# Kernel tuning notes

Measured on AMD Instinct MI355X. Metric: run time of the kernel, lower is better.

Reference implementation:

```python
import jax, jax.numpy as jnp
import numpy as np

N, F, H, E = 100000, 128, 128, 3200000
EPS = 1e-5


def setup_inputs() -> dict:
    key = jax.random.key(0)
    ks = jax.random.split(key, 16)
    g = lambda k, shape, fan_in: jax.random.normal(k, shape, jnp.float32) / np.sqrt(fan_in)
    inp = {
        'x': jax.random.normal(ks[0], (N, F), jnp.float32),
        'edge_index': jax.random.randint(ks[1], (2, E), 0, N, jnp.int64),
        # SAGEConv params: lin_l (aggregated-neighbor path, has bias), lin_r (root path, no bias)
        'W1l': g(ks[2], (F, H), F), 'b1': jnp.zeros((H,), jnp.float32), 'W1r': g(ks[3], (F, H), F),
        'W2l': g(ks[4], (H, H), H), 'b2': jnp.zeros((H,), jnp.float32), 'W2r': g(ks[5], (H, H), H),
        'W3l': g(ks[6], (H, H), H), 'b3': jnp.zeros((H,), jnp.float32), 'W3r': g(ks[7], (H, H), H),
        'W4l': g(ks[8], (H, 1), H), 'b4': jnp.zeros((1,), jnp.float32), 'W4r': g(ks[9], (H, 1), H),
        # BatchNorm affine params
        'g1': jnp.ones((H,), jnp.float32), 'be1': jnp.zeros((H,), jnp.float32),
        'g2': jnp.ones((H,), jnp.float32), 'be2': jnp.zeros((H,), jnp.float32),
        'g3': jnp.ones((H,), jnp.float32), 'be3': jnp.zeros((H,), jnp.float32),
        # shared residual linear
        'Wlin': g(ks[10], (H, H), H), 'blin': jnp.zeros((H,), jnp.float32),
    }
    return inp


def _sage(x, src, dst, Wl, b, Wr):
    # mean aggregation of source features at destination nodes
    n = x.shape[0]
    s = jax.ops.segment_sum(x[src], dst, num_segments=n)          # [N, d]
    cnt = jax.ops.segment_sum(jnp.ones_like(dst, x.dtype), dst, num_segments=n)
    agg = s / jnp.maximum(cnt, 1.0)[:, None]
    return agg @ Wl + b + x @ Wr


def _bn(x, gamma, beta):
    # training-mode batch norm over node dim (biased variance, as torch)
    mu = x.mean(0)
    var = jnp.mean((x - mu) ** 2, axis=0)
    return gamma * (x - mu) * jax.lax.rsqrt(var + EPS) + beta


def reference(x, edge_index, W1l, b1, W1r, W2l, b2, W2r, W3l, b3, W3r,
              W4l, b4, W4r, g1, be1, g2, be2, g3, be3, Wlin, blin):
    src, dst = edge_index[0], edge_index[1]
    # dropout is identity (eval-mode reference)
    x1 = jax.nn.elu(_bn(_sage(x, src, dst, W1l, b1, W1r), g1, be1))
    x2 = jax.nn.elu(_bn(_sage(x1, src, dst, W2l, b2, W2r), g2, be2))
    x2 = x2 + x1 @ Wlin + blin
    x3 = jax.nn.elu(_bn(_sage(x2, src, dst, W3l, b3, W3r), g3, be3))
    x3 = x3 + x2 @ Wlin + blin
    x4 = _sage(x3, src, dst, W4l, b4, W4r)  # [N, 1]
    return jnp.squeeze(x4, -1)
```

## Files before the change

### kernel.cpp

```cpp
#include <hip/hip_runtime.h>
#include <hip/hip_bf16.h>
#include <math.h>

#define BN_EPS 1e-5f
#define BSTRIDE 96

typedef __attribute__((ext_vector_type(8))) short bf16x8;
typedef __attribute__((ext_vector_type(4))) float f32x4;
typedef unsigned int uint32;

__device__ __forceinline__ unsigned bf16rne(float f) {
  unsigned u = __float_as_uint(f);
  unsigned r = u + 0x7fffu + ((u >> 16) & 1u);
  return r >> 16;
}
__device__ __forceinline__ float bf2f_lo(uint32 u) { return __uint_as_float(u << 16); }
__device__ __forceinline__ float bf2f_hi(uint32 u) { return __uint_as_float(u & 0xffff0000u); }
__device__ __forceinline__ uint32 packbf2(float a, float b) {
  return bf16rne(a) | (bf16rne(b) << 16);
}

__device__ __forceinline__ int edge_at(const int* __restrict__ ei, long long idx, int is64) {
  return is64 ? ei[2 * idx] : ei[idx];
}

__global__ void detect_kernel(const int* __restrict__ ei, long long E, int* __restrict__ flag) {
  __shared__ int found;
  int t = threadIdx.x;
  if (t == 0) found = 0;
  __syncthreads();
  long long npairs = E < 1024 ? E : 1024;
  for (long long p = t; p < npairs; p += blockDim.x)
    if (ei[2 * p + 1] != 0) found = 1;
  __syncthreads();
  if (t == 0) *flag = found ? 0 : 1;
}

__launch_bounds__(256)
__global__ void build_kernel(const int* __restrict__ ei, long long E,
                             const int* __restrict__ flag,
                             int* __restrict__ cnt, int* __restrict__ bkt,
                             const float* __restrict__ x, uint32* __restrict__ xb,
                             long long nf4,
                             const float* __restrict__ Wa, const float* __restrict__ Wb,
                             const float* __restrict__ Wc, const float* __restrict__ Wd,
                             const float* __restrict__ We, const float* __restrict__ Wf,
                             const float* __restrict__ Wg, ushort* __restrict__ Wp,
                             long long K3) {
  long long b = blockIdx.x;
  if (b >= K3) {
    int rb = (int)(b - K3);
    int wi = rb >> 3;
    const float* W = wi == 0 ? Wa : wi == 1 ? Wb : wi == 2 ? Wc : wi == 3 ? Wd
                   : wi == 4 ? We : wi == 5 ? Wf : Wg;
    ushort* dst = Wp + (size_t)wi * 16384;
    int s = (rb & 7) * 256 + threadIdx.x;
    int nt = s >> 8, rem = s & 255, ks = rem >> 6, lane = rem & 63;
    int q = lane >> 4, l16 = lane & 15;
    int kbase = ks * 32 + q * 8, c = nt * 16 + l16;
    uint32 o[4];
#pragma unroll
    for (int jp = 0; jp < 4; ++jp) {
      float fa = W[(size_t)(kbase + 2 * jp) * 128 + c];
      float fb = W[(size_t)(kbase + 2 * jp + 1) * 128 + c];
      o[jp] = packbf2(fa, fb);
    }
    ((uint4*)dst)[s] = make_uint4(o[0], o[1], o[2], o[3]);
    return;
  }
  int role = (int)(b % 3);
  long long id = b / 3;
  if (role == 0) {
    long long g = id * 256 + threadIdx.x;
    long long e0 = 2 * g;
    if (e0 >= E) return;
    int is64 = *flag;
    bool h1 = (e0 + 1 < E);
    int s0, s1 = 0, d0, d1 = 0;
    if (is64 && !(E & 1)) {
      int4 sv = ((const int4*)ei)[g];
      int4 dv = ((const int4*)(ei + 2 * E))[g];
      s0 = sv.x; s1 = sv.z;
      d0 = dv.x; d1 = dv.z;
    } else {
      s0 = edge_at(ei, e0, is64);
      d0 = edge_at(ei, E + e0, is64);
      if (h1) {
        s1 = edge_at(ei, e0 + 1, is64);
        d1 = edge_at(ei, E + e0 + 1, is64);
      }
    }
    int r0 = atomicAdd(&cnt[d0], 1);
    if (r0 < BSTRIDE) bkt[(size_t)d0 * BSTRIDE + r0] = s0;
    if (h1) {
      int r1 = atomicAdd(&cnt[d1], 1);
      if (r1 < BSTRIDE) bkt[(size_t)d1 * BSTRIDE + r1] = s1;
    }
  } else {
    long long i = (id * 2 + (role - 1)) * 256 + threadIdx.x;
    if (i < nf4) {
      float4 f = ((const float4*)x)[i];
      uint2 o2;
      o2.x = packbf2(f.x, f.y);
      o2.y = packbf2(f.z, f.w);
      ((uint2*)xb)[i] = o2;
    }
  }
}

__global__ void aggregate_bf16_kernel(const uint32* __restrict__ X, const int* __restrict__ cnt,
                                      const int* __restrict__ bkt, uint32* __restrict__ out,
                                      int N) {
  int gw = (int)((blockIdx.x * (long long)blockDim.x + threadIdx.x) >> 6);
  int lane = threadIdx.x & 63;
  if (gw >= N) return;
  int deg = cnt[gw];
  if (deg > BSTRIDE) deg = BSTRIDE;
  int b = gw * BSTRIDE, e = b + deg;
  int sub = lane & 15, grp = lane >> 4;
  const uint4* X4 = (const uint4*)X;
  float acc[8];
#pragma unroll
  for (int j = 0; j < 8; ++j) acc[j] = 0.f;
  for (int i = b; i < e; i += 32) {
    uint4 v[8];
#pragma unroll
    for (int u = 0; u < 8; ++u) {
      int ii = i + u * 4 + grp;
      v[u] = make_uint4(0, 0, 0, 0);
      if (ii < e) { int s = bkt[ii]; v[u] = X4[(size_t)s * 16 + sub]; }
    }
#pragma unroll
    for (int u = 0; u < 8; ++u) {
      acc[0] += bf2f_lo(v[u].x); acc[1] += bf2f_hi(v[u].x);
      acc[2] += bf2f_lo(v[u].y); acc[3] += bf2f_hi(v[u].y);
      acc[4] += bf2f_lo(v[u].z); acc[5] += bf2f_hi(v[u].z);
      acc[6] += bf2f_lo(v[u].w); acc[7] += bf2f_hi(v[u].w);
    }
  }
#pragma unroll
  for (int j = 0; j < 8; ++j) {
    acc[j] += __shfl_xor(acc[j], 16, 64);
    acc[j] += __shfl_xor(acc[j], 32, 64);
  }
  if (grp == 0) {
    float inv = 1.0f / fmaxf((float)deg, 1.0f);
    uint4 o;
    o.x = packbf2(acc[0] * inv, acc[1] * inv);
    o.y = packbf2(acc[2] * inv, acc[3] * inv);
    o.z = packbf2(acc[4] * inv, acc[5] * inv);
    o.w = packbf2(acc[6] * inv, acc[7] * inv);
    ((uint4*)out)[(size_t)gw * 16 + sub] = o;
  }
}

template <int HR>
__launch_bounds__(256)
__global__ void gemm_mfma_kernel(const ushort* __restrict__ A1, const ushort* __restrict__ W1p,
                                 const ushort* __restrict__ A2, const ushort* __restrict__ W2p,
                                 const ushort* __restrict__ W3p,
                                 const float* __restrict__ bias, const float* __restrict__ rbias,
                                 ushort* __restrict__ Y, ushort* __restrict__ R,
                                 float* __restrict__ bnsum, int N) {
  __shared__ float sred[16][128];
  int t = threadIdx.x;
  int w = t >> 6, lane = t & 63;
  int quad = lane >> 4, l16 = lane & 15;
  int row0 = blockIdx.x * 64 + w * 16;

  f32x4 accY[8], accR[HR ? 8 : 1];
#pragma unroll
  for (int nt = 0; nt < 8; ++nt) {
    accY[nt][0] = accY[nt][1] = accY[nt][2] = accY[nt][3] = 0.f;
    if (HR) {
      accR[nt][0] = accR[nt][1] = accR[nt][2] = accR[nt][3] = 0.f;
    }
  }

  int rowA = row0 + l16;
  if (rowA > N - 1) rowA = N - 1;
  const ushort* a1p = A1 + (size_t)rowA * 128 + quad * 8;
  const ushort* a2p = A2 + (size_t)rowA * 128 + quad * 8;

#pragma unroll
  for (int ks = 0; ks < 4; ++ks) {
    bf16x8 a = *(const bf16x8*)(a1p + ks * 32);
#pragma unroll
    for (int nt = 0; nt < 8; ++nt) {
      bf16x8 b = *(const bf16x8*)(W1p + ((size_t)(nt * 4 + ks) * 64 + lane) * 8);
      accY[nt] = __builtin_amdgcn_mfma_f32_16x16x32_bf16(a, b, accY[nt], 0, 0, 0);
    }
  }
#pragma unroll
  for (int ks = 0; ks < 4; ++ks) {
    bf16x8 a = *(const bf16x8*)(a2p + ks * 32);
#pragma unroll
    for (int nt = 0; nt < 8; ++nt) {
      bf16x8 b = *(const bf16x8*)(W2p + ((size_t)(nt * 4 + ks) * 64 + lane) * 8);
      accY[nt] = __builtin_amdgcn_mfma_f32_16x16x32_bf16(a, b, accY[nt], 0, 0, 0);
    }
    if (HR) {
#pragma unroll
      for (int nt = 0; nt < 8; ++nt) {
        bf16x8 b = *(const bf16x8*)(W3p + ((size_t)(nt * 4 + ks) * 64 + lane) * 8);
        accR[nt] = __builtin_amdgcn_mfma_f32_16x16x32_bf16(a, b, accR[nt], 0, 0, 0);
      }
    }
  }

  float s1v[8], s2v[8];
#pragma unroll
  for (int nt = 0; nt < 8; ++nt) {
    int c = nt * 16 + l16;
    float bv = bias[c];
    float rb = HR ? rbias[c] : 0.f;
    s1v[nt] = 0.f; s2v[nt] = 0.f;
#pragma unroll
    for (int reg = 0; reg < 4; ++reg) {
      int grow = row0 + quad * 4 + reg;
      if (grow < N) {
        float v = accY[nt][reg] + bv;
        Y[(size_t)grow * 128 + c] = (ushort)bf16rne(v);
        s1v[nt] += v; s2v[nt] += v * v;
        if (HR) {
          float vr = accR[nt][reg] + rb;
          R[(size_t)grow * 128 + c] = (ushort)bf16rne(vr);
        }
      }
    }
  }

  int rrow = w * 4 + quad;
#pragma unroll
  for (int nt = 0; nt < 8; ++nt) sred[rrow][nt * 16 + l16] = s1v[nt];
  __syncthreads();
  if (t < 128) {
    float tot = 0.f;
#pragma unroll
    for (int r16 = 0; r16 < 16; ++r16) tot += sred[r16][t];
    atomicAdd(&bnsum[(size_t)(blockIdx.x & 63) * 256 + t], tot);
  }
  __syncthreads();
#pragma unroll
  for (int nt = 0; nt < 8; ++nt) sred[rrow][nt * 16 + l16] = s2v[nt];
  __syncthreads();
  if (t < 128) {
    float tot = 0.f;
#pragma unroll
    for (int r16 = 0; r16 < 16; ++r16) tot += sred[r16][t];
    atomicAdd(&bnsum[(size_t)(blockIdx.x & 63) * 256 + 128 + t], tot);
  }
}

__global__ void bn_finalize_kernel(float* __restrict__ bnsum, float* __restrict__ bnp, int N) {
  __shared__ float part[256];
  int t = threadIdx.x;
  float a0 = 0.f, a1 = 0.f, a2 = 0.f, a3 = 0.f;
#pragma unroll
  for (int sh = 0; sh < 64; sh += 4) {
    a0 += bnsum[(size_t)(sh + 0) * 256 + t];
    a1 += bnsum[(size_t)(sh + 1) * 256 + t];
    a2 += bnsum[(size_t)(sh + 2) * 256 + t];
    a3 += bnsum[(size_t)(sh + 3) * 256 + t];
  }
  part[t] = (a0 + a1) + (a2 + a3);
  __syncthreads();
  if (t < 128) {
    float invN = 1.0f / (float)N;
    float mu = part[t] * invN;
    float var = part[128 + t] * invN - mu * mu;
    bnp[t] = mu;
    bnp[128 + t] = rsqrtf(var + BN_EPS);
  }
  __syncthreads();
  for (int i = t; i < 64 * 256; i += 256) bnsum[i] = 0.f;
}

__global__ void bn_elu_kernel(const uint4* __restrict__ Y4, const float* __restrict__ bnp,
                              const float* __restrict__ g, const float* __restrict__ be,
                              const uint4* __restrict__ res4, uint4* __restrict__ Xo4,
                              const float* __restrict__ W4l, const float* __restrict__ W4r,
                              float* __restrict__ z, float* __restrict__ rr,
                              long long total4) {
  long long i = blockIdx.x * (long long)blockDim.x + threadIdx.x;
  if (i >= total4) return;
  int c0 = (int)(i & 15) * 8;
  uint4 y = Y4[i];
  float v[8];
  {
    uint32 ww[4] = {y.x, y.y, y.z, y.w};
#pragma unroll
    for (int j = 0; j < 4; ++j) {
      int c = c0 + 2 * j;
      float e0 = g[c]     * (bf2f_lo(ww[j]) - bnp[c])     * bnp[128 + c]     + be[c];
      float e1 = g[c + 1] * (bf2f_hi(ww[j]) - bnp[c + 1]) * bnp[128 + c + 1] + be[c + 1];
      v[2 * j]     = e0 > 0.f ? e0 : expm1f(e0);
      v[2 * j + 1] = e1 > 0.f ? e1 : expm1f(e1);
    }
  }
  if (res4) {
    uint4 rv = res4[i];
    uint32 ww[4] = {rv.x, rv.y, rv.z, rv.w};
#pragma unroll
    for (int j = 0; j < 4; ++j) {
      v[2 * j]     += bf2f_lo(ww[j]);
      v[2 * j + 1] += bf2f_hi(ww[j]);
    }
  }
  if (Xo4) {
    uint4 o;
    o.x = packbf2(v[0], v[1]);
    o.y = packbf2(v[2], v[3]);
    o.z = packbf2(v[4], v[5]);
    o.w = packbf2(v[6], v[7]);
    Xo4[i] = o;
  }
  if (z) {
    float a = 0.f, bb = 0.f;
#pragma unroll
    for (int j = 0; j < 8; ++j) {
      a  += v[j] * W4l[c0 + j];
      bb += v[j] * W4r[c0 + j];
    }
    a  += __shfl_xor(a, 1, 64);  bb += __shfl_xor(bb, 1, 64);
    a  += __shfl_xor(a, 2, 64);  bb += __shfl_xor(bb, 2, 64);
    a  += __shfl_xor(a, 4, 64);  bb += __shfl_xor(bb, 4, 64);
    a  += __shfl_xor(a, 8, 64);  bb += __shfl_xor(bb, 8, 64);
    if ((i & 15) == 0) {
      long long row = i >> 4;
      z[row] = a;
      rr[row] = bb;
    }
  }
}

__global__ void final_kernel(const float* __restrict__ z, const float* __restrict__ rr,
                             const int* __restrict__ cnt, const int* __restrict__ bkt,
                             const float* __restrict__ b4, float* __restrict__ out, int N) {
  long long t = blockIdx.x * (long long)blockDim.x + threadIdx.x;
  int n = (int)(t >> 3);
  int q = (int)(t & 7);
  if (n >= N) n = N - 1;
  int deg = cnt[n];
  if (deg > BSTRIDE) deg = BSTRIDE;
  int b = n * BSTRIDE, e = b + deg;
  float s = 0.f;
  for (int i = b + q; i < e; i += 8) s += z[bkt[i]];
  s += __shfl_xor(s, 1, 64);
  s += __shfl_xor(s, 2, 64);
  s += __shfl_xor(s, 4, 64);
  if (q == 0) out[n] = s / fmaxf((float)deg, 1.0f) + b4[0] + rr[n];
}

extern "C" void kernel_launch(void* const* d_in, const int* in_sizes, int n_in,
                              void* d_out, int out_size, void* d_ws, size_t ws_size,
                              hipStream_t stream) {
  const float* x   = (const float*)d_in[0];
  const int*   ei  = (const int*)d_in[1];
  const float* W1l = (const float*)d_in[2];
  const float* b1  = (const float*)d_in[3];
  const float* W1r = (const float*)d_in[4];
  const float* W2l = (const float*)d_in[5];
  const float* b2  = (const float*)d_in[6];
  const float* W2r = (const float*)d_in[7];
  const float* W3l = (const float*)d_in[8];
  const float* b3  = (const float*)d_in[9];
  const float* W3r = (const float*)d_in[10];
  const float* W4l = (const float*)d_in[11];
  const float* b4  = (const float*)d_in[12];
  const float* W4r = (const float*)d_in[13];
  const float* g1  = (const float*)d_in[14];
  const float* be1 = (const float*)d_in[15];
  const float* g2  = (const float*)d_in[16];
  const float* be2 = (const float*)d_in[17];
  const float* g3  = (const float*)d_in[18];
  const float* be3 = (const float*)d_in[19];
  const float* Wlin= (const float*)d_in[20];
  const float* blin= (const float*)d_in[21];

  const int N = in_sizes[0] / 128;
  const long long E = in_sizes[1] / 2;
  float* out = (float*)d_out;

  const int B = 256;
  const int gb = (N + 63) / 64;

  char* w = (char*)d_ws;
  size_t o = 0;
  auto alloc = [&](size_t bytes) -> char* {
    char* p = w + o;
    o = (o + bytes + 255) & ~(size_t)255;
    return p;
  };
  int*      cnt   = (int*)alloc((size_t)N * 4);
  int*      flag  = (int*)alloc(4);
  float*    bnsum = (float*)alloc((size_t)64 * 256 * 4);
  float*    bnp   = (float*)alloc(256 * 4);
  float*    z     = (float*)alloc((size_t)N * 4);
  float*    rr    = (float*)alloc((size_t)N * 4);
  ushort*   Wp    = (ushort*)alloc((size_t)7 * 2048 * 16);
  int*      bkt   = (int*)alloc((size_t)N * BSTRIDE * 4);
  char* B1c = alloc((size_t)N * 256);
  char* B2c = alloc((size_t)N * 256);
  char* B3c = alloc((size_t)N * 256);
  (void)ws_size; (void)n_in; (void)out_size;

  uint32* B1 = (uint32*)B1c;
  uint32* B2 = (uint32*)B2c;
  uint32* B3 = (uint32*)B3c;

  const long long pairs = (E + 1) / 2;
  const int ebp = (int)((pairs + B - 1) / B);
  const long long nf4 = (long long)N * 32;
  const int cb4 = (int)((nf4 + B - 1) / B);
  int K = ebp > (cb4 + 1) / 2 ? ebp : (cb4 + 1) / 2;
  const int Gbuild = 3 * K + 56;
  const int wb = (int)(((long long)N * 64 + B - 1) / B);
  const long long tot4 = (long long)N * 16;
  const int cb = (int)((tot4 + B - 1) / B);
  const int fb = (int)(((long long)N * 8 + B - 1) / B);

  ushort* Wp1l = Wp + 0 * 16384;
  ushort* Wp1r = Wp + 1 * 16384;
  ushort* Wp2l = Wp + 2 * 16384;
  ushort* Wp2r = Wp + 3 * 16384;
  ushort* Wp3l = Wp + 4 * 16384;
  ushort* Wp3r = Wp + 5 * 16384;
  ushort* Wpln = Wp + 6 * 16384;

  hipMemsetAsync(cnt, 0, (size_t)N * 4, stream);
  hipMemsetAsync(bnsum, 0, (size_t)64 * 256 * 4, stream);
  detect_kernel<<<1, 1024, 0, stream>>>(ei, E, flag);
  build_kernel<<<Gbuild, B, 0, stream>>>(ei, E, flag, cnt, bkt, x, B2, nf4,
                                         W1l, W1r, W2l, W2r, W3l, W3r, Wlin, Wp,
                                         (long long)3 * K);

  aggregate_bf16_kernel<<<wb, B, 0, stream>>>(B2, cnt, bkt, B1, N);
  gemm_mfma_kernel<0><<<gb, B, 0, stream>>>((const ushort*)B1, Wp1l, (const ushort*)B2, Wp1r,
                                            nullptr, b1, nullptr, (ushort*)B1, nullptr,
                                            bnsum, N);
  bn_finalize_kernel<<<1, 256, 0, stream>>>(bnsum, bnp, N);
  bn_elu_kernel<<<cb, B, 0, stream>>>((const uint4*)B1, bnp, g1, be1, nullptr, (uint4*)B3,
                                      nullptr, nullptr, nullptr, nullptr, tot4);

  aggregate_bf16_kernel<<<wb, B, 0, stream>>>(B3, cnt, bkt, B1, N);
  gemm_mfma_kernel<1><<<gb, B, 0, stream>>>((const ushort*)B1, Wp2l, (const ushort*)B3, Wp2r,
                                            Wpln, b2, blin, (ushort*)B1, (ushort*)B2,
                                            bnsum, N);
  bn_finalize_kernel<<<1, 256, 0, stream>>>(bnsum, bnp, N);
  bn_elu_kernel<<<cb, B, 0, stream>>>((const uint4*)B1, bnp, g2, be2, (const uint4*)B2,
                                      (uint4*)B2, nullptr, nullptr, nullptr, nullptr, tot4);

  aggregate_bf16_kernel<<<wb, B, 0, stream>>>(B2, cnt, bkt, B1, N);
  gemm_mfma_kernel<1><<<gb, B, 0, stream>>>((const ushort*)B1, Wp3l, (const ushort*)B2, Wp3r,
                                            Wpln, b3, blin, (ushort*)B1, (ushort*)B3,
                                            bnsum, N);
  bn_finalize_kernel<<<1, 256, 0, stream>>>(bnsum, bnp, N);
  bn_elu_kernel<<<cb, B, 0, stream>>>((const uint4*)B1, bnp, g3, be3, (const uint4*)B3,
                                      nullptr, W4l, W4r, z, rr, tot4);

  final_kernel<<<fb, B, 0, stream>>>(z, rr, cnt, bkt, b4, out, N);
}
```

Measured before the change: 846.7 us.

## Fuse neighbor mean aggregation into the MFMA GEMM via swizzled LDS tile

Removes the separate aggregation kernel. Each wave of the GEMM kernel now gathers and averages neighbor features for its 16 rows and writes the bf16 means into a swizzled shared-memory tile, which feeds the MFMA A operand directly. This drops the global write and read of the aggregated matrix and three kernel launches per run, and merges the two memsets into one by reordering workspace allocation. The trade-off is less latency hiding: each wave aggregates its 16 nodes one after another before its GEMM work, with fewer waves in flight and extra LDS use, so the irregular gather may be exposed.

After: 1.252 ms. 47.9% more time.

```diff
diff --git a/kernel.cpp b/kernel.cpp
--- a/kernel.cpp
+++ b/kernel.cpp
@@ -108,66 +108,66 @@
   }
 }
 
-__global__ void aggregate_bf16_kernel(const uint32* __restrict__ X, const int* __restrict__ cnt,
-                                      const int* __restrict__ bkt, uint32* __restrict__ out,
-                                      int N) {
-  int gw = (int)((blockIdx.x * (long long)blockDim.x + threadIdx.x) >> 6);
-  int lane = threadIdx.x & 63;
-  if (gw >= N) return;
-  int deg = cnt[gw];
-  if (deg > BSTRIDE) deg = BSTRIDE;
-  int b = gw * BSTRIDE, e = b + deg;
-  int sub = lane & 15, grp = lane >> 4;
-  const uint4* X4 = (const uint4*)X;
-  float acc[8];
-#pragma unroll
-  for (int j = 0; j < 8; ++j) acc[j] = 0.f;
-  for (int i = b; i < e; i += 32) {
-    uint4 v[8];
-#pragma unroll
-    for (int u = 0; u < 8; ++u) {
-      int ii = i + u * 4 + grp;
-      v[u] = make_uint4(0, 0, 0, 0);
-      if (ii < e) { int s = bkt[ii]; v[u] = X4[(size_t)s * 16 + sub]; }
-    }
-#pragma unroll
-    for (int u = 0; u < 8; ++u) {
-      acc[0] += bf2f_lo(v[u].x); acc[1] += bf2f_hi(v[u].x);
-      acc[2] += bf2f_lo(v[u].y); acc[3] += bf2f_hi(v[u].y);
-      acc[4] += bf2f_lo(v[u].z); acc[5] += bf2f_hi(v[u].z);
-      acc[6] += bf2f_lo(v[u].w); acc[7] += bf2f_hi(v[u].w);
-    }
-  }
-#pragma unroll
-  for (int j = 0; j < 8; ++j) {
-    acc[j] += __shfl_xor(acc[j], 16, 64);
-    acc[j] += __shfl_xor(acc[j], 32, 64);
-  }
-  if (grp == 0) {
-    float inv = 1.0f / fmaxf((float)deg, 1.0f);
-    uint4 o;
-    o.x = packbf2(acc[0] * inv, acc[1] * inv);
-    o.y = packbf2(acc[2] * inv, acc[3] * inv);
-    o.z = packbf2(acc[4] * inv, acc[5] * inv);
-    o.w = packbf2(acc[6] * inv, acc[7] * inv);
-    ((uint4*)out)[(size_t)gw * 16 + sub] = o;
-  }
-}
-
 template <int HR>
 __launch_bounds__(256)
-__global__ void gemm_mfma_kernel(const ushort* __restrict__ A1, const ushort* __restrict__ W1p,
-                                 const ushort* __restrict__ A2, const ushort* __restrict__ W2p,
-                                 const ushort* __restrict__ W3p,
-                                 const float* __restrict__ bias, const float* __restrict__ rbias,
-                                 ushort* __restrict__ Y, ushort* __restrict__ R,
-                                 float* __restrict__ bnsum, int N) {
+__global__ void gemm_fused_kernel(const uint32* __restrict__ X, const int* __restrict__ cnt,
+                                  const int* __restrict__ bkt,
+                                  const ushort* __restrict__ W1p, const ushort* __restrict__ W2p,
+                                  const ushort* __restrict__ W3p,
+                                  const float* __restrict__ bias, const float* __restrict__ rbias,
+                                  ushort* __restrict__ Y, ushort* __restrict__ R,
+                                  float* __restrict__ bnsum, int N) {
   __shared__ float sred[16][128];
+  __shared__ uint32 atile[4][16 * 64];
   int t = threadIdx.x;
   int w = t >> 6, lane = t & 63;
   int quad = lane >> 4, l16 = lane & 15;
   int row0 = blockIdx.x * 64 + w * 16;
 
+  const uint4* X4 = (const uint4*)X;
+  for (int n = 0; n < 16; ++n) {
+    int node = row0 + n;
+    if (node > N - 1) node = N - 1;
+    int deg = cnt[node];
+    if (deg > BSTRIDE) deg = BSTRIDE;
+    int b = node * BSTRIDE, e = b + deg;
+    float acc[8];
+#pragma unroll
+    for (int j = 0; j < 8; ++j) acc[j] = 0.f;
+    for (int i = b; i < e; i += 32) {
+      uint4 v[8];
+#pragma unroll
+      for (int u = 0; u < 8; ++u) {
+        int ii = i + u * 4 + quad;
+        v[u] = make_uint4(0, 0, 0, 0);
+        if (ii < e) { int s = bkt[ii]; v[u] = X4[(size_t)s * 16 + l16]; }
+      }
+#pragma unroll
+      for (int u = 0; u < 8; ++u) {
+        acc[0] += bf2f_lo(v[u].x); acc[1] += bf2f_hi(v[u].x);
+        acc[2] += bf2f_lo(v[u].y); acc[3] += bf2f_hi(v[u].y);
+        acc[4] += bf2f_lo(v[u].z); acc[5] += bf2f_hi(v[u].z);
+        acc[6] += bf2f_lo(v[u].w); acc[7] += bf2f_hi(v[u].w);
+      }
+    }
+#pragma unroll
+    for (int j = 0; j < 8; ++j) {
+      acc[j] += __shfl_xor(acc[j], 16, 64);
+      acc[j] += __shfl_xor(acc[j], 32, 64);
+    }
+    if (quad == 0) {
+      float inv = 1.0f / fmaxf((float)deg, 1.0f);
+      uint4 o;
+      o.x = packbf2(acc[0] * inv, acc[1] * inv);
+      o.y = packbf2(acc[2] * inv, acc[3] * inv);
+      o.z = packbf2(acc[4] * inv, acc[5] * inv);
+      o.w = packbf2(acc[6] * inv, acc[7] * inv);
+      int off = n * 64 + ((l16 * 4) ^ ((n & 7) << 2));
+      *(uint4*)&atile[w][off] = o;
+    }
+  }
+  __syncthreads();
+
   f32x4 accY[8], accR[HR ? 8 : 1];
 #pragma unroll
   for (int nt = 0; nt < 8; ++nt) {
@@ -177,14 +177,15 @@
     }
   }
 
+  const ushort* A2 = (const ushort*)X;
   int rowA = row0 + l16;
   if (rowA > N - 1) rowA = N - 1;
-  const ushort* a1p = A1 + (size_t)rowA * 128 + quad * 8;
   const ushort* a2p = A2 + (size_t)rowA * 128 + quad * 8;
 
 #pragma unroll
   for (int ks = 0; ks < 4; ++ks) {
-    bf16x8 a = *(const bf16x8*)(a1p + ks * 32);
+    int off = l16 * 64 + ((quad * 4 + ks * 16) ^ ((l16 & 7) << 2));
+    bf16x8 a = *(const bf16x8*)&atile[w][off];
 #pragma unroll
     for (int nt = 0; nt < 8; ++nt) {
       bf16x8 b = *(const bf16x8*)(W1p + ((size_t)(nt * 4 + ks) * 64 + lane) * 8);
@@ -393,8 +394,8 @@
     return p;
   };
   int*      cnt   = (int*)alloc((size_t)N * 4);
+  float*    bnsum = (float*)alloc((size_t)64 * 256 * 4);
   int*      flag  = (int*)alloc(4);
-  float*    bnsum = (float*)alloc((size_t)64 * 256 * 4);
   float*    bnp   = (float*)alloc(256 * 4);
   float*    z     = (float*)alloc((size_t)N * 4);
   float*    rr    = (float*)alloc((size_t)N * 4);
@@ -415,7 +416,6 @@
   const int cb4 = (int)((nf4 + B - 1) / B);
   int K = ebp > (cb4 + 1) / 2 ? ebp : (cb4 + 1) / 2;
   const int Gbuild = 3 * K + 56;
-  const int wb = (int)(((long long)N * 64 + B - 1) / B);
   const long long tot4 = (long long)N * 16;
   const int cb = (int)((tot4 + B - 1) / B);
   const int fb = (int)(((long long)N * 8 + B - 1) / B);
@@ -428,33 +428,26 @@
   ushort* Wp3r = Wp + 5 * 16384;
   ushort* Wpln = Wp + 6 * 16384;
 
-  hipMemsetAsync(cnt, 0, (size_t)N * 4, stream);
-  hipMemsetAsync(bnsum, 0, (size_t)64 * 256 * 4, stream);
+  hipMemsetAsync(cnt, 0, (size_t)((char*)(bnsum + 64 * 256) - (char*)cnt), stream);
   detect_kernel<<<1, 1024, 0, stream>>>(ei, E, flag);
   build_kernel<<<Gbuild, B, 0, stream>>>(ei, E, flag, cnt, bkt, x, B2, nf4,
                                          W1l, W1r, W2l, W2r, W3l, W3r, Wlin, Wp,
                                          (long long)3 * K);
 
-  aggregate_bf16_kernel<<<wb, B, 0, stream>>>(B2, cnt, bkt, B1, N);
-  gemm_mfma_kernel<0><<<gb, B, 0, stream>>>((const ushort*)B1, Wp1l, (const ushort*)B2, Wp1r,
-                                            nullptr, b1, nullptr, (ushort*)B1, nullptr,
-                                            bnsum, N);
+  gemm_fused_kernel<0><<<gb, B, 0, stream>>>(B2, cnt, bkt, Wp1l, Wp1r, nullptr,
+                                             b1, nullptr, (ushort*)B1, nullptr, bnsum, N);
   bn_finalize_kernel<<<1, 256, 0, stream>>>(bnsum, bnp, N);
   bn_elu_kernel<<<cb, B, 0, stream>>>((const uint4*)B1, bnp, g1, be1, nullptr, (uint4*)B3,
                                       nullptr, nullptr, nullptr, nullptr, tot4);
 
-  aggregate_bf16_kernel<<<wb, B, 0, stream>>>(B3, cnt, bkt, B1, N);
-  gemm_mfma_kernel<1><<<gb, B, 0, stream>>>((const ushort*)B1, Wp2l, (const ushort*)B3, Wp2r,
-                                            Wpln, b2, blin, (ushort*)B1, (ushort*)B2,
-                                            bnsum, N);
+  gemm_fused_kernel<1><<<gb, B, 0, stream>>>(B3, cnt, bkt, Wp2l, Wp2r, Wpln,
+                                             b2, blin, (ushort*)B1, (ushort*)B2, bnsum, N);
   bn_finalize_kernel<<<1, 256, 0, stream>>>(bnsum, bnp, N);
   bn_elu_kernel<<<cb, B, 0, stream>>>((const uint4*)B1, bnp, g2, be2, (const uint4*)B2,
                                       (uint4*)B2, nullptr, nullptr, nullptr, nullptr, tot4);
 
-  aggregate_bf16_kernel<<<wb, B, 0, stream>>>(B2, cnt, bkt, B1, N);
-  gemm_mfma_kernel<1><<<gb, B, 0, stream>>>((const ushort*)B1, Wp3l, (const ushort*)B2, Wp3r,
-                                            Wpln, b3, blin, (ushort*)B1, (ushort*)B3,
-                                            bnsum, N);
+  gemm_fused_kernel<1><<<gb, B, 0, stream>>>(B2, cnt, bkt, Wp3l, Wp3r, Wpln,
+                                             b3, blin, (ushort*)B1, (ushort*)B3, bnsum, N);
   bn_finalize_kernel<<<1, 256, 0, stream>>>(bnsum, bnp, N);
   bn_elu_kernel<<<cb, B, 0, stream>>>((const uint4*)B1, bnp, g3, be3, (const uint4*)B3,
                                       nullptr, W4l, W4r, z, rr, tot4);
```
